# Optimization experiments

Measured on AMD Instinct MI355X. Metric: run time of the kernel, lower is better.

Reference implementation:

```python
import jax, jax.numpy as jnp
import numpy as np


def _attn_chunk(q, k, v, scale):
    # q: [b,s,h,d], k/v: [b,c,h,d] (one ring chunk)
    scores = jnp.einsum('bqhd,bkhd->bhqk', q, k) * scale
    lse = jax.nn.logsumexp(scores, axis=-1)            # [b,h,q]
    p = jnp.exp(scores - lse[..., None])               # [b,h,q,k]
    out = jnp.einsum('bhqk,bkhd->bqhd', p, v)          # [b,q,h,d]
    lse = jnp.transpose(lse, (0, 2, 1))[..., None]     # [b,q,h,1] for broadcast
    return out, lse


def setup_inputs() -> dict:
    key = jax.random.key(0)
    kq, kk, kv = jax.random.split(key, 3)
    B, S, H, D = 1, 4096, 16, 128
    q = jax.random.normal(kq, (B, S, H, D), dtype=jnp.float32)
    k = jax.random.normal(kk, (B, S, H, D), dtype=jnp.float32)
    v = jax.random.normal(kv, (B, S, H, D), dtype=jnp.float32)
    return {'q': q, 'k': k, 'v': v, 'ring_size': 4}


def reference(q, k, v, ring_size):
    # Ring attention forward: iterate over ring_size KV chunks, merging
    # partial (out, lse) with the sigmoid/logsigmoid online-softmax update
    # from update_out_and_lse_pass_q.
    B, S, H, D = q.shape
    R = int(ring_size)
    C = S // R
    scale = 1.0 / jnp.sqrt(jnp.asarray(D, dtype=q.dtype))
    k_chunks = k.reshape(B, R, C, H, D)
    v_chunks = v.reshape(B, R, C, H, D)

    # first ring step initializes the accumulators
    out, lse = _attn_chunk(q, k_chunks[:, 0], v_chunks[:, 0], scale)
    out = out.astype(jnp.float32)
    for r in range(1, R):
        block_out, block_lse = _attn_chunk(q, k_chunks[:, r], v_chunks[:, r], scale)
        block_out = block_out.astype(jnp.float32)
        # update_out_and_lse_pass_q
        out = out - jax.nn.sigmoid(block_lse - lse) * (out - block_out)
        lse = lse - jax.nn.log_sigmoid(lse - block_lse)
    return out
```

## Files before the change

kernel.cpp:

```cpp
#include <hip/hip_runtime.h>


#define S_LEN 4096
#define NH    16
#define DH    128
#define QT    128
#define KT    32
#define KSTR  136
#define VTS   40

typedef short bf16x8 __attribute__((ext_vector_type(8)));
typedef float floatx16 __attribute__((ext_vector_type(16)));

__device__ __forceinline__ unsigned short f2bf(float f) {
  union { float f; unsigned u; } x; x.f = f;
  unsigned r = x.u + 0x7FFFu + ((x.u >> 16) & 1u);
  return (unsigned short)(r >> 16);
}
__device__ __forceinline__ unsigned packbf(float a, float b) {
  return (unsigned)f2bf(a) | ((unsigned)f2bf(b) << 16);
}

__global__ __launch_bounds__(256) void conv_k(const float* __restrict__ Kg,
                                              unsigned short* __restrict__ Kb) {
  int idx = blockIdx.x * 256 + threadIdx.x;
  int d4 = idx & 31;
  int h  = (idx >> 5) & 15;
  int s  = idx >> 9;
  float4 a = ((const float4*)Kg)[idx];
  ushort4 o = make_ushort4(f2bf(a.x), f2bf(a.y), f2bf(a.z), f2bf(a.w));
  ((ushort4*)Kb)[(((size_t)h * S_LEN + s) << 5) + d4] = o;
}

__global__ __launch_bounds__(256) void conv_v(const float* __restrict__ Vg,
                                              unsigned short* __restrict__ Vt) {
  __shared__ unsigned short sT[DH * VTS];
  const int c = blockIdx.x;
  const int h = blockIdx.y;
  const int t = threadIdx.x;
  {
    const int key = t >> 3;
    const int d0  = (t & 7) * 16;
    const int g   = (key >> 2) & 3;
    const int pos = (key & 3) | ((((g & 1) << 1) | (g >> 1)) << 2) | (key & 16);
    const float* src = Vg + (((size_t)(c * KT + key) * NH + h) * DH + d0);
#pragma unroll
    for (int i = 0; i < 4; ++i) {
      float4 a = ((const float4*)src)[i];
      sT[(d0 + 4 * i + 0) * VTS + pos] = f2bf(a.x);
      sT[(d0 + 4 * i + 1) * VTS + pos] = f2bf(a.y);
      sT[(d0 + 4 * i + 2) * VTS + pos] = f2bf(a.z);
      sT[(d0 + 4 * i + 3) * VTS + pos] = f2bf(a.w);
    }
  }
  __syncthreads();
  {
    const int d = t >> 1, hf = t & 1;
    uint4 w0 = *(const uint4*)&sT[d * VTS + hf * 16];
    uint4 w1 = *(const uint4*)&sT[d * VTS + hf * 16 + 8];
    size_t ob = ((size_t)(h * DH + d)) * S_LEN + c * KT + hf * 16;
    *(uint4*)&Vt[ob]     = w0;
    *(uint4*)&Vt[ob + 8] = w1;
  }
}

__global__ __launch_bounds__(256, 3) void fa_fwd2(
    const float* __restrict__ Qg, const unsigned short* __restrict__ Kb,
    const unsigned short* __restrict__ Vt, float* __restrict__ Og) {
  __shared__ unsigned short sK[KT * KSTR];
  __shared__ unsigned short sVT[DH * VTS];

  const int tid  = threadIdx.x;
  const int lane = tid & 63;
  const int wave = tid >> 6;
  const int f   = blockIdx.x;
  const int i   = f >> 3;
  const int h   = (f & 7) + 8 * (i & 1);
  const int q0  = (i >> 1) * QT;

  bf16x8 qf[8];
  {
    const float* qr = Qg +
        ((size_t)(q0 + wave * 32 + (lane & 31)) * NH + h) * DH + (lane >> 5) * 8;
#pragma unroll
    for (int kc = 0; kc < 8; ++kc) {
      float4 a = *(const float4*)(qr + kc * 16);
      float4 b = *(const float4*)(qr + kc * 16 + 4);
      bf16x8 q;
      q[0] = f2bf(a.x); q[1] = f2bf(a.y); q[2] = f2bf(a.z); q[3] = f2bf(a.w);
      q[4] = f2bf(b.x); q[5] = f2bf(b.y); q[6] = f2bf(b.z); q[7] = f2bf(b.w);
      qf[kc] = q;
    }
  }

  floatx16 oacc[4];
#pragma unroll
  for (int dt = 0; dt < 4; ++dt)
#pragma unroll
    for (int j = 0; j < 16; ++j) oacc[dt][j] = 0.f;
  float ssum = 0.f;

  const unsigned short* Kh = Kb + (size_t)h * S_LEN * DH;
  const unsigned short* Vh = Vt + (size_t)h * DH * S_LEN;

  for (int kt = 0; kt < S_LEN; kt += KT) {
    __syncthreads();
    {
      const int key = tid >> 3, seg = tid & 7;
      const unsigned short* g = Kh + (size_t)(kt + key) * DH + seg * 16;
      uint4 a = ((const uint4*)g)[0];
      uint4 b = ((const uint4*)g)[1];
      unsigned short* dst = &sK[key * KSTR + seg * 16];
      *(uint4*)dst       = a;
      *(uint4*)(dst + 8) = b;
    }
    {
      const int d = tid >> 1, hf = tid & 1;
      const unsigned short* g = Vh + (size_t)d * S_LEN + kt + hf * 16;
      uint4 a = ((const uint4*)g)[0];
      uint4 b = ((const uint4*)g)[1];
      unsigned short* dst = &sVT[d * VTS + hf * 16];
      *(uint4*)dst       = a;
      *(uint4*)(dst + 8) = b;
    }
    __syncthreads();

    floatx16 sc;
#pragma unroll
    for (int j = 0; j < 16; ++j) sc[j] = 0.f;
    {
      const unsigned short* kb = &sK[(lane & 31) * KSTR + ((lane >> 5) * 8)];
#pragma unroll
      for (int kc = 0; kc < 8; ++kc) {
        bf16x8 kf = *(const bf16x8*)(kb + kc * 16);
        sc = __builtin_amdgcn_mfma_f32_32x32x16_bf16(kf, qf[kc], sc, 0, 0, 0);
      }
    }

    float p[16];
#pragma unroll
    for (int j = 0; j < 16; ++j) {
      p[j] = __expf(sc[j] * 0.08838834764831845f);
      ssum += p[j];
    }
    bf16x8 pf0, pf1;
    {
      unsigned* u0 = (unsigned*)&pf0;
      unsigned* u1 = (unsigned*)&pf1;
#pragma unroll
      for (int m = 0; m < 4; ++m) {
        u0[m] = packbf(p[2 * m], p[2 * m + 1]);
        u1[m] = packbf(p[8 + 2 * m], p[9 + 2 * m]);
      }
    }

    {
      const unsigned short* vb = &sVT[(lane & 31) * VTS + ((lane >> 5) * 8)];
#pragma unroll
      for (int dt = 0; dt < 4; ++dt) {
        bf16x8 v0 = *(const bf16x8*)(vb + dt * 32 * VTS);
        bf16x8 v1 = *(const bf16x8*)(vb + dt * 32 * VTS + 16);
        oacc[dt] = __builtin_amdgcn_mfma_f32_32x32x16_bf16(pf0, v0, oacc[dt], 0, 0, 0);
        oacc[dt] = __builtin_amdgcn_mfma_f32_32x32x16_bf16(pf1, v1, oacc[dt], 0, 0, 0);
      }
    }
  }

  float tot  = ssum + __shfl_xor(ssum, 32);
  float vinv = 1.0f / tot;
  const int col = lane & 31;
  const int rb  = (lane >> 5) * 4;
#pragma unroll
  for (int j = 0; j < 16; ++j) {
    const int row = (j & 3) + 8 * (j >> 2) + rb;
    const float inv = __shfl(vinv, row);
    float* op = Og + ((size_t)(q0 + wave * 32 + row) * NH + h) * DH + col;
#pragma unroll
    for (int dt = 0; dt < 4; ++dt) op[dt * 32] = oacc[dt][j] * inv;
  }
}

#define QSTR  136
#define PSTR  40
__global__ __launch_bounds__(256, 2) void fa_fwd_v1(
    const float* __restrict__ Qg, const float* __restrict__ Kg,
    const float* __restrict__ Vg, float* __restrict__ Og)
{
  __shared__ unsigned short sQ[QT * QSTR];
  __shared__ unsigned short sK1[KT * KSTR];
  __shared__ unsigned short sVT1[DH * VTS];
  __shared__ unsigned short sP[4][32 * PSTR];
  const int tid  = threadIdx.x;
  const int lane = tid & 63;
  const int wave = tid >> 6;
  const int h    = blockIdx.y;
  const int q0   = blockIdx.x * QT;
  {
    const int row = tid >> 1;
    const int db  = (tid & 1) * 64;
    const float* gq = Qg + ((size_t)(q0 + row) * NH + h) * DH + db;
    unsigned short* dst = &sQ[row * QSTR + db];
#pragma unroll
    for (int i = 0; i < 16; ++i) {
      float4 a = ((const float4*)gq)[i];
      *(ushort4*)(dst + 4 * i) =
          make_ushort4(f2bf(a.x), f2bf(a.y), f2bf(a.z), f2bf(a.w));
    }
  }
  __syncthreads();
  bf16x8 qf[8];
  {
    const unsigned short* qr =
        &sQ[(wave * 32 + (lane & 31)) * QSTR + ((lane >> 5) * 8)];
#pragma unroll
    for (int kc = 0; kc < 8; ++kc) qf[kc] = *(const bf16x8*)(qr + kc * 16);
  }
  floatx16 oacc[4];
  float sl[16];
#pragma unroll
  for (int j = 0; j < 16; ++j) sl[j] = 0.f;
#pragma unroll
  for (int dt = 0; dt < 4; ++dt)
#pragma unroll
    for (int j = 0; j < 16; ++j) oacc[dt][j] = 0.f;
  for (int kt = 0; kt < S_LEN; kt += KT) {
    __syncthreads();
    {
      const int key = tid >> 3;
      const int db  = (tid & 7) * 16;
      const float* gk = Kg + ((size_t)(kt + key) * NH + h) * DH + db;
      unsigned short* dst = &sK1[key * KSTR + db];
#pragma unroll
      for (int i = 0; i < 4; ++i) {
        float4 a = ((const float4*)gk)[i];
        *(ushort4*)(dst + 4 * i) =
            make_ushort4(f2bf(a.x), f2bf(a.y), f2bf(a.z), f2bf(a.w));
      }
    }
    {
      const int kp = tid & 15;
      const int db = (tid >> 4) * 8;
      const float* g0 = Vg + ((size_t)(kt + 2 * kp) * NH + h) * DH + db;
      const float* g1 = g0 + (size_t)NH * DH;
      float4 a0 = ((const float4*)g0)[0], b0 = ((const float4*)g0)[1];
      float4 a1 = ((const float4*)g1)[0], b1 = ((const float4*)g1)[1];
      float e0[8] = {a0.x, a0.y, a0.z, a0.w, b0.x, b0.y, b0.z, b0.w};
      float e1[8] = {a1.x, a1.y, a1.z, a1.w, b1.x, b1.y, b1.z, b1.w};
      unsigned* dw = (unsigned*)sVT1;
#pragma unroll
      for (int j = 0; j < 8; ++j)
        dw[(db + j) * (VTS / 2) + kp] =
            (unsigned)f2bf(e0[j]) | ((unsigned)f2bf(e1[j]) << 16);
    }
    __syncthreads();
    floatx16 sc;
#pragma unroll
    for (int j = 0; j < 16; ++j) sc[j] = 0.f;
    {
      const unsigned short* kb = &sK1[(lane & 31) * KSTR + ((lane >> 5) * 8)];
#pragma unroll
      for (int kc = 0; kc < 8; ++kc) {
        bf16x8 bf = *(const bf16x8*)(kb + kc * 16);
        sc = __builtin_amdgcn_mfma_f32_32x32x16_bf16(qf[kc], bf, sc, 0, 0, 0);
      }
    }
    unsigned short pw[16];
#pragma unroll
    for (int j = 0; j < 16; ++j) {
      float p = __expf(sc[j] * 0.08838834764831845f);
      sl[j] += p;
      pw[j] = f2bf(p);
    }
    {
      unsigned short* pb = sP[wave];
      const int col = lane & 31;
      const int rb  = (lane >> 5) * 4;
#pragma unroll
      for (int j = 0; j < 16; ++j) {
        const int row = (j & 3) + 8 * (j >> 2) + rb;
        pb[row * PSTR + col] = pw[j];
      }
    }
    __syncthreads();
    bf16x8 pf0, pf1;
    {
      const unsigned short* pr =
          &sP[wave][(lane & 31) * PSTR + ((lane >> 5) * 8)];
      pf0 = *(const bf16x8*)(pr);
      pf1 = *(const bf16x8*)(pr + 16);
    }
#pragma unroll
    for (int dt = 0; dt < 4; ++dt) {
      const unsigned short* vb =
          &sVT1[(dt * 32 + (lane & 31)) * VTS + ((lane >> 5) * 8)];
      bf16x8 v0 = *(const bf16x8*)(vb);
      bf16x8 v1 = *(const bf16x8*)(vb + 16);
      oacc[dt] = __builtin_amdgcn_mfma_f32_32x32x16_bf16(pf0, v0, oacc[dt], 0, 0, 0);
      oacc[dt] = __builtin_amdgcn_mfma_f32_32x32x16_bf16(pf1, v1, oacc[dt], 0, 0, 0);
    }
  }
#pragma unroll
  for (int j = 0; j < 16; ++j) {
    float s = sl[j];
    s += __shfl_xor(s, 1);
    s += __shfl_xor(s, 2);
    s += __shfl_xor(s, 4);
    s += __shfl_xor(s, 8);
    s += __shfl_xor(s, 16);
    sl[j] = 1.0f / s;
  }
  {
    const int col = lane & 31;
    const int rb  = (lane >> 5) * 4;
#pragma unroll
    for (int j = 0; j < 16; ++j) {
      const int row = (j & 3) + 8 * (j >> 2) + rb;
      float* op = Og + ((size_t)(q0 + wave * 32 + row) * NH + h) * DH + col;
#pragma unroll
      for (int dt = 0; dt < 4; ++dt)
        op[dt * 32] = oacc[dt][j] * sl[j];
    }
  }
}

extern "C" void kernel_launch(void* const* d_in, const int* in_sizes, int n_in,
                              void* d_out, int out_size, void* d_ws, size_t ws_size,
                              hipStream_t stream) {
  const float* q = (const float*)d_in[0];
  const float* k = (const float*)d_in[1];
  const float* v = (const float*)d_in[2];
  float* o = (float*)d_out;
  const size_t elems = (size_t)NH * S_LEN * DH;
  const size_t need  = 2 * elems * sizeof(unsigned short);
  if (ws_size >= need) {
    unsigned short* Kb = (unsigned short*)d_ws;
    unsigned short* Vt = Kb + elems;
    conv_k<<<(int)(elems / 4 / 256), 256, 0, stream>>>(k, Kb);
    conv_v<<<dim3(S_LEN / KT, NH), 256, 0, stream>>>(v, Vt);
    fa_fwd2<<<512, 256, 0, stream>>>(q, Kb, Vt, o);
  } else {
    fa_fwd_v1<<<dim3(S_LEN / QT, NH), 256, 0, stream>>>(q, k, v, o);
  }
}
```

Baseline: 291.4 us.

## Double-buffer K/V tiles with direct global-to-LDS loads and XOR swizzle

Replaces the register-staged, single-buffered K/V tile loads with global_load_lds DMA into two ping-pong LDS buffers, so the next tile streams in while the current one is computed. Padded LDS strides are replaced by XOR-swizzled layouts with precomputed read offsets to avoid bank conflicts. P is converted to bf16 by truncation instead of rounding, and a constant bias is folded into the exponent via fmaf. Occupancy is lowered from 3 to 2 blocks per CU, and truncation slightly changes numerics.

```diff
diff --git a/kernel.cpp b/kernel.cpp
--- a/kernel.cpp
+++ b/kernel.cpp
@@ -8,6 +8,8 @@
 #define KT    32
 #define KSTR  136
 #define VTS   40
+#define QSTR  136
+#define PSTR  40
 
 typedef short bf16x8 __attribute__((ext_vector_type(8)));
 typedef float floatx16 __attribute__((ext_vector_type(16)));
@@ -17,8 +19,11 @@
   unsigned r = x.u + 0x7FFFu + ((x.u >> 16) & 1u);
   return (unsigned short)(r >> 16);
 }
-__device__ __forceinline__ unsigned packbf(float a, float b) {
-  return (unsigned)f2bf(a) | ((unsigned)f2bf(b) << 16);
+
+__device__ __forceinline__ void gll16(const unsigned short* g, unsigned short* l) {
+  __builtin_amdgcn_global_load_lds(
+      (const __attribute__((address_space(1))) void*)g,
+      (__attribute__((address_space(3))) void*)l, 16, 0, 0);
 }
 
 __global__ __launch_bounds__(256) void conv_k(const float* __restrict__ Kg,
@@ -64,24 +69,55 @@
   }
 }
 
-__global__ __launch_bounds__(256, 3) void fa_fwd2(
+__global__ __launch_bounds__(256, 2) void fa_fwd3(
     const float* __restrict__ Qg, const unsigned short* __restrict__ Kb,
     const unsigned short* __restrict__ Vt, float* __restrict__ Og) {
-  __shared__ unsigned short sK[KT * KSTR];
-  __shared__ unsigned short sVT[DH * VTS];
+  __shared__ __align__(16) unsigned short sK[2][4096];
+  __shared__ __align__(16) unsigned short sV[2][4096];
 
   const int tid  = threadIdx.x;
   const int lane = tid & 63;
   const int wave = tid >> 6;
-  const int f   = blockIdx.x;
-  const int i   = f >> 3;
-  const int h   = (f & 7) + 8 * (i & 1);
-  const int q0  = (i >> 1) * QT;
+  const int f  = blockIdx.x;
+  const int i  = f >> 3;
+  const int h  = (f & 7) + 8 * (i & 1);
+  const int q0 = (i >> 1) * QT;
+
+  const unsigned short* Kh = Kb + (size_t)h * S_LEN * DH;
+  const unsigned short* Vh = Vt + (size_t)h * DH * S_LEN;
+
+  int skoff[2], svoff[2];
+#pragma unroll
+  for (int s = 0; s < 2; ++s) {
+    const int ii = wave * 2 + s;
+    { const int C = ii * 64 + lane;
+      const int m = C >> 4;
+      const int j = (lane & 15) ^ (m & 15);
+      skoff[s] = m * DH + j * 8; }
+    { const int C = ii * 64 + lane;
+      const int r = C >> 2;
+      const int j = (lane & 3) ^ ((r >> 1) & 3);
+      svoff[s] = r * S_LEN + j * 8; }
+  }
+  const int ldst = wave * 1024;
+
+  const int m31 = lane & 31, hh = lane >> 5;
+  int kro[8], vro[8];
+#pragma unroll
+  for (int kc = 0; kc < 8; ++kc)
+    kro[kc] = m31 * 128 + (((2 * kc + hh) ^ (m31 & 15)) * 8);
+#pragma unroll
+  for (int dt = 0; dt < 4; ++dt)
+#pragma unroll
+    for (int ff = 0; ff < 2; ++ff) {
+      const int r = dt * 32 + m31;
+      vro[dt * 2 + ff] = r * 32 + (((2 * ff + hh) ^ ((r >> 1) & 3)) * 8);
+    }
 
   bf16x8 qf[8];
   {
     const float* qr = Qg +
-        ((size_t)(q0 + wave * 32 + (lane & 31)) * NH + h) * DH + (lane >> 5) * 8;
+        ((size_t)(q0 + wave * 32 + m31) * NH + h) * DH + hh * 8;
 #pragma unroll
     for (int kc = 0; kc < 8; ++kc) {
       float4 a = *(const float4*)(qr + kc * 16);
@@ -100,88 +136,72 @@
     for (int j = 0; j < 16; ++j) oacc[dt][j] = 0.f;
   float ssum = 0.f;
 
-  const unsigned short* Kh = Kb + (size_t)h * S_LEN * DH;
-  const unsigned short* Vh = Vt + (size_t)h * DH * S_LEN;
-
-  for (int kt = 0; kt < S_LEN; kt += KT) {
-    __syncthreads();
-    {
-      const int key = tid >> 3, seg = tid & 7;
-      const unsigned short* g = Kh + (size_t)(kt + key) * DH + seg * 16;
-      uint4 a = ((const uint4*)g)[0];
-      uint4 b = ((const uint4*)g)[1];
-      unsigned short* dst = &sK[key * KSTR + seg * 16];
-      *(uint4*)dst       = a;
-      *(uint4*)(dst + 8) = b;
-    }
-    {
-      const int d = tid >> 1, hf = tid & 1;
-      const unsigned short* g = Vh + (size_t)d * S_LEN + kt + hf * 16;
-      uint4 a = ((const uint4*)g)[0];
-      uint4 b = ((const uint4*)g)[1];
-      unsigned short* dst = &sVT[d * VTS + hf * 16];
-      *(uint4*)dst       = a;
-      *(uint4*)(dst + 8) = b;
-    }
-    __syncthreads();
-
-    floatx16 sc;
-#pragma unroll
-    for (int j = 0; j < 16; ++j) sc[j] = 0.f;
-    {
-      const unsigned short* kb = &sK[(lane & 31) * KSTR + ((lane >> 5) * 8)];
-#pragma unroll
-      for (int kc = 0; kc < 8; ++kc) {
-        bf16x8 kf = *(const bf16x8*)(kb + kc * 16);
-        sc = __builtin_amdgcn_mfma_f32_32x32x16_bf16(kf, qf[kc], sc, 0, 0, 0);
-      }
-    }
-
-    float p[16];
-#pragma unroll
-    for (int j = 0; j < 16; ++j) {
-      p[j] = __expf(sc[j] * 0.08838834764831845f);
-      ssum += p[j];
-    }
-    bf16x8 pf0, pf1;
-    {
-      unsigned* u0 = (unsigned*)&pf0;
-      unsigned* u1 = (unsigned*)&pf1;
-#pragma unroll
-      for (int m = 0; m < 4; ++m) {
-        u0[m] = packbf(p[2 * m], p[2 * m + 1]);
-        u1[m] = packbf(p[8 + 2 * m], p[9 + 2 * m]);
-      }
-    }
-
-    {
-      const unsigned short* vb = &sVT[(lane & 31) * VTS + ((lane >> 5) * 8)];
-#pragma unroll
-      for (int dt = 0; dt < 4; ++dt) {
-        bf16x8 v0 = *(const bf16x8*)(vb + dt * 32 * VTS);
-        bf16x8 v1 = *(const bf16x8*)(vb + dt * 32 * VTS + 16);
-        oacc[dt] = __builtin_amdgcn_mfma_f32_32x32x16_bf16(pf0, v0, oacc[dt], 0, 0, 0);
-        oacc[dt] = __builtin_amdgcn_mfma_f32_32x32x16_bf16(pf1, v1, oacc[dt], 0, 0, 0);
-      }
-    }
-  }
+#define ISSUE(BK, BV, KTV)                                                    \
+  {                                                                           \
+    _Pragma("unroll") for (int s = 0; s < 2; ++s) {                           \
+      gll16(Kh + (size_t)(KTV) * DH + skoff[s], &(BK)[ldst + s * 512]);       \
+      gll16(Vh + (KTV) + svoff[s], &(BV)[ldst + s * 512]);                    \
+    }                                                                         \
+  }
+
+#define COMPUTE_TILE(KB, VB)                                                  \
+  {                                                                           \
+    floatx16 sc;                                                              \
+    _Pragma("unroll") for (int j = 0; j < 16; ++j) sc[j] = 0.f;               \
+    _Pragma("unroll") for (int kc = 0; kc < 8; ++kc) {                        \
+      bf16x8 kf = *(const bf16x8*)((KB) + kro[kc]);                           \
+      sc = __builtin_amdgcn_mfma_f32_32x32x16_bf16(kf, qf[kc], sc, 0, 0, 0);  \
+    }                                                                         \
+    float p[16];                                                              \
+    _Pragma("unroll") for (int j = 0; j < 16; ++j) {                          \
+      p[j] = __expf(fmaf(sc[j], 0.08838834764831845f, 0.0019512177f));        \
+      ssum += p[j];                                                           \
+    }                                                                         \
+    bf16x8 pf0, pf1;                                                          \
+    unsigned* u0 = (unsigned*)&pf0;                                           \
+    unsigned* u1 = (unsigned*)&pf1;                                           \
+    _Pragma("unroll") for (int m = 0; m < 4; ++m) {                           \
+      u0[m] = (__float_as_uint(p[2 * m + 1]) & 0xFFFF0000u) |                 \
+              (__float_as_uint(p[2 * m]) >> 16);                              \
+      u1[m] = (__float_as_uint(p[2 * m + 9]) & 0xFFFF0000u) |                 \
+              (__float_as_uint(p[2 * m + 8]) >> 16);                          \
+    }                                                                         \
+    _Pragma("unroll") for (int dt = 0; dt < 4; ++dt) {                        \
+      bf16x8 v0 = *(const bf16x8*)((VB) + vro[dt * 2]);                       \
+      bf16x8 v1 = *(const bf16x8*)((VB) + vro[dt * 2 + 1]);                   \
+      oacc[dt] =                                                              \
+          __builtin_amdgcn_mfma_f32_32x32x16_bf16(pf0, v0, oacc[dt], 0, 0, 0);\
+      oacc[dt] =                                                              \
+          __builtin_amdgcn_mfma_f32_32x32x16_bf16(pf1, v1, oacc[dt], 0, 0, 0);\
+    }                                                                         \
+  }
+
+  ISSUE(sK[0], sV[0], 0);
+  __syncthreads();
+  for (int t = 0; t < 64; ++t) {
+    ISSUE(sK[1], sV[1], 64 * t + 32);
+    COMPUTE_TILE(sK[0], sV[0]);
+    __syncthreads();
+    if (t < 63) ISSUE(sK[0], sV[0], 64 * t + 64);
+    COMPUTE_TILE(sK[1], sV[1]);
+    __syncthreads();
+  }
+#undef ISSUE
+#undef COMPUTE_TILE
 
   float tot  = ssum + __shfl_xor(ssum, 32);
   float vinv = 1.0f / tot;
-  const int col = lane & 31;
-  const int rb  = (lane >> 5) * 4;
+  const int rb = hh * 4;
 #pragma unroll
   for (int j = 0; j < 16; ++j) {
     const int row = (j & 3) + 8 * (j >> 2) + rb;
     const float inv = __shfl(vinv, row);
-    float* op = Og + ((size_t)(q0 + wave * 32 + row) * NH + h) * DH + col;
+    float* op = Og + ((size_t)(q0 + wave * 32 + row) * NH + h) * DH + m31;
 #pragma unroll
     for (int dt = 0; dt < 4; ++dt) op[dt * 32] = oacc[dt][j] * inv;
   }
 }
 
-#define QSTR  136
-#define PSTR  40
 __global__ __launch_bounds__(256, 2) void fa_fwd_v1(
     const float* __restrict__ Qg, const float* __restrict__ Kg,
     const float* __restrict__ Vg, float* __restrict__ Og)
@@ -337,7 +357,7 @@
     unsigned short* Vt = Kb + elems;
     conv_k<<<(int)(elems / 4 / 256), 256, 0, stream>>>(k, Kb);
     conv_v<<<dim3(S_LEN / KT, NH), 256, 0, stream>>>(v, Vt);
-    fa_fwd2<<<512, 256, 0, stream>>>(q, Kb, Vt, o);
+    fa_fwd3<<<512, 256, 0, stream>>>(q, Kb, Vt, o);
   } else {
     fa_fwd_v1<<<dim3(S_LEN / QT, NH), 256, 0, stream>>>(q, k, v, o);
   }
```

Result: faster. 277.2 us (-4.9%).
